# Kernel optimization log

Hardware: AMD Instinct MI355X
Metric: run time of the kernel (lower is better)

The kernel has to match this reference:

```python
import jax, jax.numpy as jnp
import numpy as np

INPUT, LATENT, HIDDEN, LAYERS = 64, 32, 128, 1
N, L = 256, 512


def setup_inputs() -> dict:
    key = jax.random.key(0)
    ks = jax.random.split(key, 12)
    s = 0.02
    inp = {
        "X": jax.random.normal(ks[0], (N, L, INPUT), jnp.float32),
        "eps_z": jax.random.normal(ks[1], (L, LAYERS, N, LATENT), jnp.float32),
        "eps_x": jax.random.normal(ks[2], (L, LAYERS, N, INPUT), jnp.float32),
        # qzcx: NormalModel(input+hidden -> latent): Linear to (mean, raw_std)
        "Wq": s * jax.random.normal(ks[3], (INPUT + HIDDEN, 2 * LATENT), jnp.float32),
        "bq": jnp.zeros((2 * LATENT,), jnp.float32),
        # pxcz: NormalModel(latent+hidden -> input)
        "Wp": s * jax.random.normal(ks[4], (LATENT + HIDDEN, 2 * INPUT), jnp.float32),
        "bp": jnp.zeros((2 * INPUT,), jnp.float32),
        # GRUCell(input+latent -> hidden), gates ordered (r, z, n) as in torch
        "W_ih": s * jax.random.normal(ks[5], (INPUT + LATENT, 3 * HIDDEN), jnp.float32),
        "W_hh": s * jax.random.normal(ks[6], (HIDDEN, 3 * HIDDEN), jnp.float32),
        "b_ih": jnp.zeros((3 * HIDDEN,), jnp.float32),
        "b_hh": jnp.zeros((3 * HIDDEN,), jnp.float32),
    }
    return inp


def _normal(x, W, b):
    # Linear head producing (mean, std) with softplus-positive std
    out = x @ W + b
    mean, raw = jnp.split(out, 2, axis=-1)
    return mean, jax.nn.softplus(raw)


def _gru(xcat, h, W_ih, W_hh, b_ih, b_hh):
    gi = xcat @ W_ih + b_ih
    gh = h @ W_hh + b_hh
    gi_r, gi_z, gi_n = jnp.split(gi, 3, axis=-1)
    gh_r, gh_z, gh_n = jnp.split(gh, 3, axis=-1)
    r = jax.nn.sigmoid(gi_r + gh_r)
    z = jax.nn.sigmoid(gi_z + gh_z)
    n = jnp.tanh(gi_n + r * gh_n)
    return (1.0 - z) * n + z * h


def reference(X, eps_z, eps_x, Wq, bq, Wp, bp, W_ih, W_hh, b_ih, b_hh):
    # X: [N, L, input] (batch_first). Recurrence over L via lax.scan.
    Xt = jnp.transpose(X, (1, 0, 2))  # [L, N, input]

    def cell(x, h, ez, ex):
        # one VRNNCell step (eval path); x:[N,In], h:[N,H]
        inf_mean, inf_std = _normal(jnp.concatenate([x, h], -1), Wq, bq)
        z_gen = inf_mean + inf_std * ez  # rsample
        x_mean, x_std = _normal(jnp.concatenate([z_gen, h], -1), Wp, bp)
        x_gen = x_mean + x_std * ex  # rsample
        return _gru(jnp.concatenate([x_gen, z_gen], -1), h, W_ih, W_hh, b_ih, b_hh)

    cell_layers = jax.vmap(cell, in_axes=(None, 0, 0, 0))  # over layer dim

    def step(hs, inputs):
        x, ez, ex = inputs
        new_hs = cell_layers(x, hs, ez, ex)  # [LAYERS, N, H]
        return new_hs, new_hs[-1]

    h0 = jnp.zeros((LAYERS, X.shape[0], HIDDEN), X.dtype)
    hs_final, outs = jax.lax.scan(step, h0, (Xt, eps_z, eps_x))
    output = jnp.transpose(outs, (1, 0, 2))  # [N, L, H] (batch_first)
    return output, hs_final
```

## Files before the change

### kernel.cpp

```cpp
#include <hip/hip_runtime.h>

namespace {

constexpr int NROWS = 256, LSTEPS = 512, IN = 64, LAT = 32, HID = 128;

typedef _Float16 h2 __attribute__((ext_vector_type(2)));
typedef _Float16 h8 __attribute__((ext_vector_type(8)));

__device__ __forceinline__ float fast_sigmoid(float x) {
    return __fdividef(1.f, 1.f + __expf(-x));
}
__device__ __forceinline__ float fast_softplus(float x) {
    return fmaxf(x, 0.f) + log1pf(__expf(-fabsf(x)));
}
__device__ __forceinline__ float fast_tanh(float x) {
    float e = __expf(-2.f * fabsf(x));
    float t = __fdividef(1.f - e, 1.f + e);
    return copysignf(t, x);
}

__device__ __forceinline__ float dot2f(h2 w, h2 a, float c) {
#if __has_builtin(__builtin_amdgcn_fdot2)
    return __builtin_amdgcn_fdot2(w, a, c, false);
#else
    return fmaf((float)w[0], (float)a[0], fmaf((float)w[1], (float)a[1], c));
#endif
}

__device__ __forceinline__ h2 packw(float a, float b) {
    h2 r; r[0] = (_Float16)a; r[1] = (_Float16)b; return r;
}

template<int BASE, int NPAIR>
__device__ __forceinline__ float dotp2(const _Float16* act, const h2 (&w)[120]) {
    float a0 = 0.f, a1 = 0.f, a2 = 0.f, a3 = 0.f;
#pragma unroll
    for (int i = 0; i < NPAIR / 4; ++i) {
        h8 blk = *(const h8*)(act + 8 * i);
        a0 = dot2f(w[BASE + 4 * i + 0], __builtin_shufflevector(blk, blk, 0, 1), a0);
        a1 = dot2f(w[BASE + 4 * i + 1], __builtin_shufflevector(blk, blk, 2, 3), a1);
        a2 = dot2f(w[BASE + 4 * i + 2], __builtin_shufflevector(blk, blk, 4, 5), a2);
        a3 = dot2f(w[BASE + 4 * i + 3], __builtin_shufflevector(blk, blk, 6, 7), a3);
    }
    return (a0 + a1) + (a2 + a3);
}

}

__global__ __launch_bounds__(512)
__attribute__((amdgpu_waves_per_eu(2, 2)))
void vrnn_kernel(
    const float* __restrict__ X, const float* __restrict__ EZ, const float* __restrict__ EX,
    const float* __restrict__ Wq, const float* __restrict__ bq,
    const float* __restrict__ Wp, const float* __restrict__ bp,
    const float* __restrict__ Wih, const float* __restrict__ Whh,
    const float* __restrict__ bih, const float* __restrict__ bhh,
    float* __restrict__ out)
{
    __shared__ alignas(16) _Float16 XH[192];
    __shared__ alignas(16) _Float16 ZH[160];
    __shared__ alignas(16) _Float16 XZ[96];
    __shared__ alignas(16) float q_part[64][4];
    __shared__ alignas(16) float p_part[128][2];
    __shared__ alignas(16) float gi_part[384][2];
    __shared__ alignas(16) float gh_part[384][2];

    const int t = threadIdx.x;
    const int n = blockIdx.x;

    h2 wpk[120];

    if (t < 256) {
        {
            const int m = t >> 2, k0 = (t & 3) * 48;
#pragma unroll
            for (int j = 0; j < 24; ++j) { int k = k0 + 2 * j;
                wpk[j] = packw(Wq[k * 64 + m], Wq[(k + 1) * 64 + m]); }
        }
        {
            const int m = t >> 1, k0 = (t & 1) * 80;
#pragma unroll
            for (int j = 0; j < 40; ++j) { int k = k0 + 2 * j;
                wpk[24 + j] = packw(Wp[k * 128 + m], Wp[(k + 1) * 128 + m]); }
        }
        {
            const int m = t;
#pragma unroll
            for (int j = 0; j < 48; ++j) { int k = 2 * j;
                wpk[64 + j] = packw(Wih[k * 384 + m], Wih[(k + 1) * 384 + m]); }
        }
    } else {
        const int y = t - 256;
        const int mo = y >> 1, k0 = (y & 1) * 64;
#pragma unroll
        for (int s = 0; s < 3; ++s) {
            const int m = s * 128 + mo;
#pragma unroll
            for (int j = 0; j < 32; ++j) { int k = k0 + 2 * j;
                wpk[s * 32 + j] = packw(Whh[k * 384 + m], Whh[(k + 1) * 384 + m]); }
        }
        {
            const int m = 256 + mo, kg = (y & 1) * 48;
#pragma unroll
            for (int j = 0; j < 24; ++j) { int k = kg + 2 * j;
                wpk[96 + j] = packw(Wih[k * 384 + m], Wih[(k + 1) * 384 + m]); }
        }
    }

    float bz0 = 0.f, bz1 = 0.f, bx0 = 0.f, bx1 = 0.f;
    float bir = 0.f, biz = 0.f, bin_ = 0.f, bhr = 0.f, bhz = 0.f, bhn = 0.f;
    if (t < 32)  { bz0 = bq[t]; bz1 = bq[t + 32]; }
    if (t < 64)  { bx0 = bp[t]; bx1 = bp[t + 64]; }
    if (t < 128) { bir = bih[t]; biz = bih[128 + t]; bin_ = bih[256 + t];
                   bhr = bhh[t]; bhz = bhh[128 + t]; bhn = bhh[256 + t]; }

    const float* Xrow = X + n * (LSTEPS * IN);
    float* orow = out + n * (LSTEPS * HID);
    float hreg = 0.f;
    if (t < 128) { XH[64 + t] = (_Float16)0.f; ZH[32 + t] = (_Float16)0.f; }
    if (t < 64)  XH[t] = (_Float16)Xrow[t];
    float ez_nxt = (t < 32) ? EZ[n * LAT + t] : 0.f;
    float ex_nxt = (t < 64) ? EX[n * IN + t]  : 0.f;
    float xn_nxt = 0.f;
    __syncthreads();

    for (int l = 0; l < LSTEPS; ++l) {
        const float ez_cur = ez_nxt, ex_cur = ex_nxt;
        if (l + 1 < LSTEPS) {
            if (t < 32) ez_nxt = EZ[(l + 1) * (NROWS * LAT) + n * LAT + t];
            if (t < 64) { ex_nxt = EX[(l + 1) * (NROWS * IN) + n * IN + t];
                          xn_nxt = Xrow[(l + 1) * IN + t]; }
        }

        if (t < 256) {
            const int m = t >> 2, ks = t & 3;
            q_part[m][ks] = dotp2<0, 24>(XH + ks * 48, wpk);
        } else {
            const int y = t - 256;
            gh_part[y >> 1][y & 1] = dotp2<0, 32>(XH + 64 + (y & 1) * 64, wpk);
        }
        __syncthreads();

        if (t < 32) {
            float4 qm = *(const float4*)q_part[t];
            float4 qr = *(const float4*)q_part[t + 32];
            float mean = (qm.x + qm.y) + (qm.z + qm.w) + bz0;
            float raw  = (qr.x + qr.y) + (qr.z + qr.w) + bz1;
            float z = fmaf(fast_softplus(raw), ez_cur, mean);
            ZH[t] = (_Float16)z; XZ[64 + t] = (_Float16)z;
        }
        __syncthreads();

        if (t < 256) {
            const int m = t >> 1, ks = t & 1;
            p_part[m][ks] = dotp2<24, 40>(ZH + ks * 80, wpk);
        } else {
            const int y = t - 256;
            gh_part[128 + (y >> 1)][y & 1] = dotp2<32, 32>(XH + 64 + (y & 1) * 64, wpk);
        }
        __syncthreads();

        if (t < 64) {
            float mean = p_part[t][0] + p_part[t][1] + bx0;
            float raw  = p_part[t + 64][0] + p_part[t + 64][1] + bx1;
            float xg = fmaf(fast_softplus(raw), ex_cur, mean);
            XZ[t] = (_Float16)xg;
        }
        __syncthreads();

        if (t < 256) {
            gi_part[t][0] = dotp2<64, 48>(XZ, wpk);
            if (t < 64 && l + 1 < LSTEPS) XH[t] = (_Float16)xn_nxt;
        } else {
            const int y = t - 256;
            gh_part[256 + (y >> 1)][y & 1] = dotp2<64, 32>(XH + 64 + (y & 1) * 64, wpk);
            gi_part[256 + (y >> 1)][y & 1] = dotp2<96, 24>(XZ + (y & 1) * 48, wpk);
        }
        __syncthreads();

        if (t < 128) {
            float gir = gi_part[t][0] + bir;
            float giz = gi_part[128 + t][0] + biz;
            float gin = gi_part[256 + t][0] + gi_part[256 + t][1] + bin_;
            float ghr = gh_part[t][0] + gh_part[t][1] + bhr;
            float ghz = gh_part[128 + t][0] + gh_part[128 + t][1] + bhz;
            float ghn = gh_part[256 + t][0] + gh_part[256 + t][1] + bhn;
            float r  = fast_sigmoid(gir + ghr);
            float zg = fast_sigmoid(giz + ghz);
            float nn = fast_tanh(fmaf(r, ghn, gin));
            float hnew = fmaf(zg, hreg - nn, nn);
            hreg = hnew;
            _Float16 hf = (_Float16)hnew;
            XH[64 + t] = hf; ZH[32 + t] = hf;
            orow[l * HID + t] = hnew;
        }
        __syncthreads();
    }

    if (t < 128) out[NROWS * LSTEPS * HID + n * HID + t] = hreg;
}

extern "C" void kernel_launch(void* const* d_in, const int* in_sizes, int n_in,
                              void* d_out, int out_size, void* d_ws, size_t ws_size,
                              hipStream_t stream) {
    const float* X   = (const float*)d_in[0];
    const float* EZ  = (const float*)d_in[1];
    const float* EX  = (const float*)d_in[2];
    const float* Wq  = (const float*)d_in[3];
    const float* bq  = (const float*)d_in[4];
    const float* Wp  = (const float*)d_in[5];
    const float* bp  = (const float*)d_in[6];
    const float* Wih = (const float*)d_in[7];
    const float* Whh = (const float*)d_in[8];
    const float* bih = (const float*)d_in[9];
    const float* bhh = (const float*)d_in[10];
    float* out = (float*)d_out;

    vrnn_kernel<<<dim3(NROWS), dim3(512), 0, stream>>>(
        X, EZ, EX, Wq, bq, Wp, bp, Wih, Whh, bih, bhh, out);
}
```

Before: 952.1 us.

## Reassign per-thread work to cut barriers and reduce heads via wave shuffles

Redistributes the weight slices across the 512 threads so the W_hh product is split evenly between both halves, and the h-part of the p-head is computed early alongside q. The q and p head reductions now use __shfl_xor inside a wave instead of shared-memory partial arrays, which removes two of the six barriers per timestep. The GRU input gates are split by the z and x contributions so they can be computed in separate phases. In exchange, gate accumulation needs more partial sums per output and the register-resident weight mapping becomes more complex.

```diff
diff --git a/kernel.cpp b/kernel.cpp
--- a/kernel.cpp
+++ b/kernel.cpp
@@ -32,15 +32,15 @@
 }
 
 template<int BASE, int NPAIR>
-__device__ __forceinline__ float dotp2(const _Float16* act, const h2 (&w)[120]) {
-    float a0 = 0.f, a1 = 0.f, a2 = 0.f, a3 = 0.f;
+__device__ __forceinline__ float dotp2(const _Float16* act, const h2 (&w)[120], float init) {
+    float a0 = init, a1 = 0.f, a2 = 0.f, a3 = 0.f;
 #pragma unroll
     for (int i = 0; i < NPAIR / 4; ++i) {
-        h8 blk = *(const h8*)(act + 8 * i);
-        a0 = dot2f(w[BASE + 4 * i + 0], __builtin_shufflevector(blk, blk, 0, 1), a0);
-        a1 = dot2f(w[BASE + 4 * i + 1], __builtin_shufflevector(blk, blk, 2, 3), a1);
-        a2 = dot2f(w[BASE + 4 * i + 2], __builtin_shufflevector(blk, blk, 4, 5), a2);
-        a3 = dot2f(w[BASE + 4 * i + 3], __builtin_shufflevector(blk, blk, 6, 7), a3);
+        h8 b = *(const h8*)(act + 8 * i);
+        a0 = dot2f(w[BASE + 4 * i + 0], __builtin_shufflevector(b, b, 0, 1), a0);
+        a1 = dot2f(w[BASE + 4 * i + 1], __builtin_shufflevector(b, b, 2, 3), a1);
+        a2 = dot2f(w[BASE + 4 * i + 2], __builtin_shufflevector(b, b, 4, 5), a2);
+        a3 = dot2f(w[BASE + 4 * i + 3], __builtin_shufflevector(b, b, 6, 7), a3);
     }
     return (a0 + a1) + (a2 + a3);
 }
@@ -58,140 +58,178 @@
     float* __restrict__ out)
 {
     __shared__ alignas(16) _Float16 XH[192];
-    __shared__ alignas(16) _Float16 ZH[160];
-    __shared__ alignas(16) _Float16 XZ[96];
-    __shared__ alignas(16) float q_part[64][4];
-    __shared__ alignas(16) float p_part[128][2];
-    __shared__ alignas(16) float gi_part[384][2];
-    __shared__ alignas(16) float gh_part[384][2];
+    __shared__ alignas(16) _Float16 ZH[32];
+    __shared__ alignas(16) _Float16 XZ[64];
+    __shared__ alignas(16) float gh_part[384][4];
+    __shared__ alignas(16) float gi_part[384][8];
 
     const int t = threadIdx.x;
     const int n = blockIdx.x;
 
     h2 wpk[120];
 
+    const int y = t - 256;
+
+    int mg[3], kqg[3];
+    int mx[3], kqx[3];
+    int mz[3], khz[3];
+#pragma unroll
+    for (int i = 0; i < 3; ++i) {
+        int s = (t < 256) ? (3 * t + i) : (768 + 3 * y + i);
+        mg[i] = s >> 2; kqg[i] = s & 3;
+        mx[i] = s >> 2; kqx[i] = s & 3;
+        if (t >= 256) { int sz = 3 * y + i; mz[i] = sz >> 1; khz[i] = sz & 1; }
+        else { mz[i] = 0; khz[i] = 0; }
+    }
+
     if (t < 256) {
-        {
-            const int m = t >> 2, k0 = (t & 3) * 48;
-#pragma unroll
-            for (int j = 0; j < 24; ++j) { int k = k0 + 2 * j;
-                wpk[j] = packw(Wq[k * 64 + m], Wq[(k + 1) * 64 + m]); }
-        }
-        {
-            const int m = t >> 1, k0 = (t & 1) * 80;
-#pragma unroll
-            for (int j = 0; j < 40; ++j) { int k = k0 + 2 * j;
-                wpk[24 + j] = packw(Wp[k * 128 + m], Wp[(k + 1) * 128 + m]); }
-        }
-        {
-            const int m = t;
-#pragma unroll
-            for (int j = 0; j < 48; ++j) { int k = 2 * j;
-                wpk[64 + j] = packw(Wih[k * 384 + m], Wih[(k + 1) * 384 + m]); }
-        }
+        const int j = t >> 2, sub = t & 3;
+        const int o = (sub < 2) ? j : j + 64;
+        const int kh = sub & 1;
+#pragma unroll
+        for (int p = 0; p < 32; ++p) { int k = 32 + 64 * kh + 2 * p;
+            wpk[p] = packw(Wp[k * 128 + o], Wp[(k + 1) * 128 + o]); }
+#pragma unroll
+        for (int p = 0; p < 8; ++p) { int k = 16 * kh + 2 * p;
+            wpk[32 + p] = packw(Wp[k * 128 + o], Wp[(k + 1) * 128 + o]); }
+#pragma unroll
+        for (int i = 0; i < 3; ++i)
+#pragma unroll
+            for (int p = 0; p < 16; ++p) { int k = 32 * kqg[i] + 2 * p;
+                wpk[40 + 16 * i + p] = packw(Whh[k * 384 + mg[i]], Whh[(k + 1) * 384 + mg[i]]); }
+#pragma unroll
+        for (int i = 0; i < 3; ++i)
+#pragma unroll
+            for (int p = 0; p < 8; ++p) { int k = 16 * kqx[i] + 2 * p;
+                wpk[88 + 8 * i + p] = packw(Wih[k * 384 + mx[i]], Wih[(k + 1) * 384 + mx[i]]); }
     } else {
-        const int y = t - 256;
-        const int mo = y >> 1, k0 = (y & 1) * 64;
-#pragma unroll
-        for (int s = 0; s < 3; ++s) {
-            const int m = s * 128 + mo;
-#pragma unroll
-            for (int j = 0; j < 32; ++j) { int k = k0 + 2 * j;
-                wpk[s * 32 + j] = packw(Whh[k * 384 + m], Whh[(k + 1) * 384 + m]); }
-        }
-        {
-            const int m = 256 + mo, kg = (y & 1) * 48;
-#pragma unroll
-            for (int j = 0; j < 24; ++j) { int k = kg + 2 * j;
-                wpk[96 + j] = packw(Wih[k * 384 + m], Wih[(k + 1) * 384 + m]); }
-        }
-    }
-
-    float bz0 = 0.f, bz1 = 0.f, bx0 = 0.f, bx1 = 0.f;
+        const int j = y >> 3, sub = y & 7;
+        const int o = (sub < 4) ? j : j + 32;
+        const int k0 = (sub & 3) * 48;
+#pragma unroll
+        for (int p = 0; p < 24; ++p) { int k = k0 + 2 * p;
+            wpk[p] = packw(Wq[k * 64 + o], Wq[(k + 1) * 64 + o]); }
+#pragma unroll
+        for (int i = 0; i < 3; ++i)
+#pragma unroll
+            for (int p = 0; p < 16; ++p) { int k = 32 * kqg[i] + 2 * p;
+                wpk[24 + 16 * i + p] = packw(Whh[k * 384 + mg[i]], Whh[(k + 1) * 384 + mg[i]]); }
+#pragma unroll
+        for (int i = 0; i < 3; ++i)
+#pragma unroll
+            for (int p = 0; p < 8; ++p) { int k = 64 + 16 * khz[i] + 2 * p;
+                wpk[72 + 8 * i + p] = packw(Wih[k * 384 + mz[i]], Wih[(k + 1) * 384 + mz[i]]); }
+#pragma unroll
+        for (int i = 0; i < 3; ++i)
+#pragma unroll
+            for (int p = 0; p < 8; ++p) { int k = 16 * kqx[i] + 2 * p;
+                wpk[96 + 8 * i + p] = packw(Wih[k * 384 + mx[i]], Wih[(k + 1) * 384 + mx[i]]); }
+    }
+
+    float bqm = 0.f, bqr = 0.f, bpm = 0.f, bpr = 0.f;
     float bir = 0.f, biz = 0.f, bin_ = 0.f, bhr = 0.f, bhz = 0.f, bhn = 0.f;
-    if (t < 32)  { bz0 = bq[t]; bz1 = bq[t + 32]; }
-    if (t < 64)  { bx0 = bp[t]; bx1 = bp[t + 64]; }
+    if (t >= 256 && (y & 7) == 0) { bqm = bq[y >> 3]; bqr = bq[(y >> 3) + 32]; }
+    if (t < 256 && (t & 3) == 0)  { bpm = bp[t >> 2]; bpr = bp[(t >> 2) + 64]; }
     if (t < 128) { bir = bih[t]; biz = bih[128 + t]; bin_ = bih[256 + t];
                    bhr = bhh[t]; bhz = bhh[128 + t]; bhn = bhh[256 + t]; }
 
     const float* Xrow = X + n * (LSTEPS * IN);
     float* orow = out + n * (LSTEPS * HID);
     float hreg = 0.f;
-    if (t < 128) { XH[64 + t] = (_Float16)0.f; ZH[32 + t] = (_Float16)0.f; }
+    if (t < 128) XH[64 + t] = (_Float16)0.f;
     if (t < 64)  XH[t] = (_Float16)Xrow[t];
-    float ez_nxt = (t < 32) ? EZ[n * LAT + t] : 0.f;
-    float ex_nxt = (t < 64) ? EX[n * IN + t]  : 0.f;
-    float xn_nxt = 0.f;
+
+    float ez_nxt = 0.f, ex_nxt = 0.f, xn_nxt = 0.f;
+    if (t >= 256 && (y & 7) == 0) ez_nxt = EZ[n * LAT + (y >> 3)];
+    if (t < 256 && (t & 3) == 0)  ex_nxt = EX[n * IN + (t >> 2)];
     __syncthreads();
+
+    float ph = 0.f;
 
     for (int l = 0; l < LSTEPS; ++l) {
         const float ez_cur = ez_nxt, ex_cur = ex_nxt;
         if (l + 1 < LSTEPS) {
-            if (t < 32) ez_nxt = EZ[(l + 1) * (NROWS * LAT) + n * LAT + t];
-            if (t < 64) { ex_nxt = EX[(l + 1) * (NROWS * IN) + n * IN + t];
-                          xn_nxt = Xrow[(l + 1) * IN + t]; }
+            if (t >= 256 && (y & 7) == 0) ez_nxt = EZ[(l + 1) * (NROWS * LAT) + n * LAT + (y >> 3)];
+            if (t < 256 && (t & 3) == 0)  ex_nxt = EX[(l + 1) * (NROWS * IN) + n * IN + (t >> 2)];
+            if (t < 64) xn_nxt = Xrow[(l + 1) * IN + t];
         }
 
         if (t < 256) {
-            const int m = t >> 2, ks = t & 3;
-            q_part[m][ks] = dotp2<0, 24>(XH + ks * 48, wpk);
+            const int kh = t & 1;
+            ph = dotp2<0, 32>(XH + 64 + 64 * kh, wpk, 0.f);
+            float g0 = dotp2<40, 16>(XH + 64 + 32 * kqg[0], wpk, 0.f);
+            float g1 = dotp2<56, 16>(XH + 64 + 32 * kqg[1], wpk, 0.f);
+            float g2 = dotp2<72, 16>(XH + 64 + 32 * kqg[2], wpk, 0.f);
+            gh_part[mg[0]][kqg[0]] = g0;
+            gh_part[mg[1]][kqg[1]] = g1;
+            gh_part[mg[2]][kqg[2]] = g2;
         } else {
-            const int y = t - 256;
-            gh_part[y >> 1][y & 1] = dotp2<0, 32>(XH + 64 + (y & 1) * 64, wpk);
-        }
-        __syncthreads();
-
-        if (t < 32) {
-            float4 qm = *(const float4*)q_part[t];
-            float4 qr = *(const float4*)q_part[t + 32];
-            float mean = (qm.x + qm.y) + (qm.z + qm.w) + bz0;
-            float raw  = (qr.x + qr.y) + (qr.z + qr.w) + bz1;
-            float z = fmaf(fast_softplus(raw), ez_cur, mean);
-            ZH[t] = (_Float16)z; XZ[64 + t] = (_Float16)z;
+            const int sub = y & 7, k0 = (sub & 3) * 48;
+            float q = dotp2<0, 24>(XH + k0, wpk, 0.f);
+            float g0 = dotp2<24, 16>(XH + 64 + 32 * kqg[0], wpk, 0.f);
+            float g1 = dotp2<40, 16>(XH + 64 + 32 * kqg[1], wpk, 0.f);
+            float g2 = dotp2<56, 16>(XH + 64 + 32 * kqg[2], wpk, 0.f);
+            gh_part[mg[0]][kqg[0]] = g0;
+            gh_part[mg[1]][kqg[1]] = g1;
+            gh_part[mg[2]][kqg[2]] = g2;
+            q += __shfl_xor(q, 1);
+            q += __shfl_xor(q, 2);
+            float other = __shfl_xor(q, 4);
+            if (sub == 0) {
+                float z = (q + bqm) + fast_softplus(other + bqr) * ez_cur;
+                ZH[y >> 3] = (_Float16)z;
+            }
         }
         __syncthreads();
 
         if (t < 256) {
-            const int m = t >> 1, ks = t & 1;
-            p_part[m][ks] = dotp2<24, 40>(ZH + ks * 80, wpk);
+            const int kh = t & 1, sub = t & 3;
+            float tot = dotp2<32, 8>(ZH + 16 * kh, wpk, ph);
+            tot += __shfl_xor(tot, 1);
+            float other = __shfl_xor(tot, 2);
+            if (sub == 0) {
+                float xg = (tot + bpm) + fast_softplus(other + bpr) * ex_cur;
+                XZ[t >> 2] = (_Float16)xg;
+            }
         } else {
-            const int y = t - 256;
-            gh_part[128 + (y >> 1)][y & 1] = dotp2<32, 32>(XH + 64 + (y & 1) * 64, wpk);
-        }
-        __syncthreads();
-
-        if (t < 64) {
-            float mean = p_part[t][0] + p_part[t][1] + bx0;
-            float raw  = p_part[t + 64][0] + p_part[t + 64][1] + bx1;
-            float xg = fmaf(fast_softplus(raw), ex_cur, mean);
-            XZ[t] = (_Float16)xg;
+            gi_part[mz[0]][khz[0]] = dotp2<72, 8>(ZH + 16 * khz[0], wpk, 0.f);
+            gi_part[mz[1]][khz[1]] = dotp2<80, 8>(ZH + 16 * khz[1], wpk, 0.f);
+            gi_part[mz[2]][khz[2]] = dotp2<88, 8>(ZH + 16 * khz[2], wpk, 0.f);
         }
         __syncthreads();
 
         if (t < 256) {
-            gi_part[t][0] = dotp2<64, 48>(XZ, wpk);
+            gi_part[mx[0]][2 + kqx[0]] = dotp2<88, 8>(XZ + 16 * kqx[0], wpk, 0.f);
+            gi_part[mx[1]][2 + kqx[1]] = dotp2<96, 8>(XZ + 16 * kqx[1], wpk, 0.f);
+            gi_part[mx[2]][2 + kqx[2]] = dotp2<104, 8>(XZ + 16 * kqx[2], wpk, 0.f);
             if (t < 64 && l + 1 < LSTEPS) XH[t] = (_Float16)xn_nxt;
         } else {
-            const int y = t - 256;
-            gh_part[256 + (y >> 1)][y & 1] = dotp2<64, 32>(XH + 64 + (y & 1) * 64, wpk);
-            gi_part[256 + (y >> 1)][y & 1] = dotp2<96, 24>(XZ + (y & 1) * 48, wpk);
+            gi_part[mx[0]][2 + kqx[0]] = dotp2<96, 8>(XZ + 16 * kqx[0], wpk, 0.f);
+            gi_part[mx[1]][2 + kqx[1]] = dotp2<104, 8>(XZ + 16 * kqx[1], wpk, 0.f);
+            gi_part[mx[2]][2 + kqx[2]] = dotp2<112, 8>(XZ + 16 * kqx[2], wpk, 0.f);
         }
         __syncthreads();
 
         if (t < 128) {
-            float gir = gi_part[t][0] + bir;
-            float giz = gi_part[128 + t][0] + biz;
-            float gin = gi_part[256 + t][0] + gi_part[256 + t][1] + bin_;
-            float ghr = gh_part[t][0] + gh_part[t][1] + bhr;
-            float ghz = gh_part[128 + t][0] + gh_part[128 + t][1] + bhz;
-            float ghn = gh_part[256 + t][0] + gh_part[256 + t][1] + bhn;
+            float4 a; float2 b2;
+            a = *(const float4*)&gi_part[t][0];        b2 = *(const float2*)&gi_part[t][4];
+            float gir = (a.x + a.y) + (a.z + a.w) + (b2.x + b2.y) + bir;
+            a = *(const float4*)&gi_part[128 + t][0];  b2 = *(const float2*)&gi_part[128 + t][4];
+            float giz = (a.x + a.y) + (a.z + a.w) + (b2.x + b2.y) + biz;
+            a = *(const float4*)&gi_part[256 + t][0];  b2 = *(const float2*)&gi_part[256 + t][4];
+            float gin = (a.x + a.y) + (a.z + a.w) + (b2.x + b2.y) + bin_;
+            a = *(const float4*)&gh_part[t][0];
+            float ghr = (a.x + a.y) + (a.z + a.w) + bhr;
+            a = *(const float4*)&gh_part[128 + t][0];
+            float ghz = (a.x + a.y) + (a.z + a.w) + bhz;
+            a = *(const float4*)&gh_part[256 + t][0];
+            float ghn = (a.x + a.y) + (a.z + a.w) + bhn;
             float r  = fast_sigmoid(gir + ghr);
             float zg = fast_sigmoid(giz + ghz);
             float nn = fast_tanh(fmaf(r, ghn, gin));
             float hnew = fmaf(zg, hreg - nn, nn);
             hreg = hnew;
-            _Float16 hf = (_Float16)hnew;
-            XH[64 + t] = hf; ZH[32 + t] = hf;
+            XH[64 + t] = (_Float16)hnew;
             orow[l * HID + t] = hnew;
         }
         __syncthreads();
```

After: 1.023 ms. 1.07x slower.

## Split VRNN step across 1024 threads with shuffle reductions and fewer barriers

Applied to the files above, without the earlier changes.

Doubles the block to 1024 threads and repartitions the per-step work. One half computes the hidden-to-hidden GRU products, while the other half computes the q, p and input-gate products, splitting the p and gi dot products into h-dependent and z/x-dependent parts so they can overlap. Partial sums are reduced with cross-lane shuffles instead of shared-memory staging arrays, which cuts the barriers per step from six to four. It also swaps __syncthreads for a raw s_waitcnt+s_barrier and uses a cheaper softplus log. The risk is higher register pressure with 1024 threads, and the hand-written barrier relies on its lgkmcnt wait to order the shared-memory writes.

```diff
diff --git a/kernel.cpp b/kernel.cpp
--- a/kernel.cpp
+++ b/kernel.cpp
@@ -11,45 +11,48 @@
     return __fdividef(1.f, 1.f + __expf(-x));
 }
 __device__ __forceinline__ float fast_softplus(float x) {
-    return fmaxf(x, 0.f) + log1pf(__expf(-fabsf(x)));
+    return fmaxf(x, 0.f) + __logf(1.f + __expf(-fabsf(x)));
 }
 __device__ __forceinline__ float fast_tanh(float x) {
     float e = __expf(-2.f * fabsf(x));
-    float t = __fdividef(1.f - e, 1.f + e);
-    return copysignf(t, x);
-}
-
-__device__ __forceinline__ float dot2f(h2 w, h2 a, float c) {
-#if __has_builtin(__builtin_amdgcn_fdot2)
+    return copysignf(__fdividef(1.f - e, 1.f + e), x);
+}
+__device__ __forceinline__ float dot2(h2 w, h2 a, float c) {
     return __builtin_amdgcn_fdot2(w, a, c, false);
-#else
-    return fmaf((float)w[0], (float)a[0], fmaf((float)w[1], (float)a[1], c));
-#endif
-}
-
+}
 __device__ __forceinline__ h2 packw(float a, float b) {
     h2 r; r[0] = (_Float16)a; r[1] = (_Float16)b; return r;
 }
-
-template<int BASE, int NPAIR>
-__device__ __forceinline__ float dotp2(const _Float16* act, const h2 (&w)[120]) {
-    float a0 = 0.f, a1 = 0.f, a2 = 0.f, a3 = 0.f;
-#pragma unroll
-    for (int i = 0; i < NPAIR / 4; ++i) {
-        h8 blk = *(const h8*)(act + 8 * i);
-        a0 = dot2f(w[BASE + 4 * i + 0], __builtin_shufflevector(blk, blk, 0, 1), a0);
-        a1 = dot2f(w[BASE + 4 * i + 1], __builtin_shufflevector(blk, blk, 2, 3), a1);
-        a2 = dot2f(w[BASE + 4 * i + 2], __builtin_shufflevector(blk, blk, 4, 5), a2);
-        a3 = dot2f(w[BASE + 4 * i + 3], __builtin_shufflevector(blk, blk, 6, 7), a3);
-    }
-    return (a0 + a1) + (a2 + a3);
-}
-
-}
-
-__global__ __launch_bounds__(512)
-__attribute__((amdgpu_waves_per_eu(2, 2)))
-void vrnn_kernel(
+__device__ __forceinline__ void soft_barrier() {
+    asm volatile("s_waitcnt lgkmcnt(0)\n\ts_barrier" ::: "memory");
+}
+template<int NB>
+__device__ __forceinline__ void load_acts(const _Float16* p, h2* o) {
+#pragma unroll
+    for (int i = 0; i < NB; ++i) {
+        h8 b = *(const h8*)(p + 8 * i);
+        o[4*i+0] = __builtin_shufflevector(b, b, 0, 1);
+        o[4*i+1] = __builtin_shufflevector(b, b, 2, 3);
+        o[4*i+2] = __builtin_shufflevector(b, b, 4, 5);
+        o[4*i+3] = __builtin_shufflevector(b, b, 6, 7);
+    }
+}
+template<int NP>
+__device__ __forceinline__ float dotw(const h2* w, const h2* a, float init) {
+    float s0 = init, s1 = 0.f, s2 = 0.f, s3 = 0.f;
+#pragma unroll
+    for (int i = 0; i < NP / 4; ++i) {
+        s0 = dot2(w[4*i+0], a[4*i+0], s0);
+        s1 = dot2(w[4*i+1], a[4*i+1], s1);
+        s2 = dot2(w[4*i+2], a[4*i+2], s2);
+        s3 = dot2(w[4*i+3], a[4*i+3], s3);
+    }
+    return (s0 + s1) + (s2 + s3);
+}
+
+}
+
+__global__ __launch_bounds__(1024) void vrnn_kernel(
     const float* __restrict__ X, const float* __restrict__ EZ, const float* __restrict__ EX,
     const float* __restrict__ Wq, const float* __restrict__ bq,
     const float* __restrict__ Wp, const float* __restrict__ bp,
@@ -58,146 +61,168 @@
     float* __restrict__ out)
 {
     __shared__ alignas(16) _Float16 XH[192];
-    __shared__ alignas(16) _Float16 ZH[160];
-    __shared__ alignas(16) _Float16 XZ[96];
-    __shared__ alignas(16) float q_part[64][4];
-    __shared__ alignas(16) float p_part[128][2];
-    __shared__ alignas(16) float gi_part[384][2];
-    __shared__ alignas(16) float gh_part[384][2];
-
-    const int t = threadIdx.x;
-    const int n = blockIdx.x;
-
-    h2 wpk[120];
-
-    if (t < 256) {
-        {
-            const int m = t >> 2, k0 = (t & 3) * 48;
-#pragma unroll
-            for (int j = 0; j < 24; ++j) { int k = k0 + 2 * j;
-                wpk[j] = packw(Wq[k * 64 + m], Wq[(k + 1) * 64 + m]); }
-        }
-        {
-            const int m = t >> 1, k0 = (t & 1) * 80;
-#pragma unroll
-            for (int j = 0; j < 40; ++j) { int k = k0 + 2 * j;
-                wpk[24 + j] = packw(Wp[k * 128 + m], Wp[(k + 1) * 128 + m]); }
-        }
-        {
-            const int m = t;
-#pragma unroll
-            for (int j = 0; j < 48; ++j) { int k = 2 * j;
-                wpk[64 + j] = packw(Wih[k * 384 + m], Wih[(k + 1) * 384 + m]); }
+    __shared__ alignas(16) _Float16 ZH[32];
+    __shared__ alignas(16) _Float16 XZ[64];
+    __shared__ alignas(16) float GIR[128][4];
+
+    const int t = threadIdx.x, n = blockIdx.x;
+    const bool isG = (t < 512);
+    const int e = t - 512;
+
+    h2 wpk[80];
+
+    float bh0=0,bh1=0,bh2=0,bi0=0,bi1=0,bi2=0;
+    float bqm=0,bqr=0,bpm=0,bpr=0;
+    float hprev = 0.f;
+
+    if (isG) {
+        const int u = t >> 2, q = t & 3;
+#pragma unroll
+        for (int g = 0; g < 3; ++g)
+#pragma unroll
+            for (int p = 0; p < 16; ++p) {
+                int k = 32*q + 2*p;
+                wpk[g*16+p] = packw(Whh[k*384 + g*128 + u], Whh[(k+1)*384 + g*128 + u]);
+            }
+        if (q == 0) {
+            bh0 = bhh[u]; bh1 = bhh[128+u]; bh2 = bhh[256+u];
+            bi0 = bih[u]; bi1 = bih[128+u]; bi2 = bih[256+u];
         }
     } else {
-        const int y = t - 256;
-        const int mo = y >> 1, k0 = (y & 1) * 64;
-#pragma unroll
-        for (int s = 0; s < 3; ++s) {
-            const int m = s * 128 + mo;
-#pragma unroll
-            for (int j = 0; j < 32; ++j) { int k = k0 + 2 * j;
-                wpk[s * 32 + j] = packw(Whh[k * 384 + m], Whh[(k + 1) * 384 + m]); }
-        }
-        {
-            const int m = 256 + mo, kg = (y & 1) * 48;
-#pragma unroll
-            for (int j = 0; j < 24; ++j) { int k = kg + 2 * j;
-                wpk[96 + j] = packw(Wih[k * 384 + m], Wih[(k + 1) * 384 + m]); }
-        }
-    }
-
-    float bz0 = 0.f, bz1 = 0.f, bx0 = 0.f, bx1 = 0.f;
-    float bir = 0.f, biz = 0.f, bin_ = 0.f, bhr = 0.f, bhz = 0.f, bhn = 0.f;
-    if (t < 32)  { bz0 = bq[t]; bz1 = bq[t + 32]; }
-    if (t < 64)  { bx0 = bp[t]; bx1 = bp[t + 64]; }
-    if (t < 128) { bir = bih[t]; biz = bih[128 + t]; bin_ = bih[256 + t];
-                   bhr = bhh[t]; bhz = bhh[128 + t]; bhn = bhh[256 + t]; }
-
-    const float* Xrow = X + n * (LSTEPS * IN);
-    float* orow = out + n * (LSTEPS * HID);
-    float hreg = 0.f;
-    if (t < 128) { XH[64 + t] = (_Float16)0.f; ZH[32 + t] = (_Float16)0.f; }
-    if (t < 64)  XH[t] = (_Float16)Xrow[t];
-    float ez_nxt = (t < 32) ? EZ[n * LAT + t] : 0.f;
-    float ex_nxt = (t < 64) ? EX[n * IN + t]  : 0.f;
-    float xn_nxt = 0.f;
+        const int lane8 = e & 7, mr = (e >> 2) & 1, kq = e & 3;
+        const int xu8 = e >> 3, gu = e >> 2;
+        const int o = xu8 + mr * 64;
+#pragma unroll
+        for (int p = 0; p < 16; ++p) { int k = 32 + 32*kq + 2*p;
+            wpk[p] = packw(Wp[k*128+o], Wp[(k+1)*128+o]); }
+#pragma unroll
+        for (int p = 0; p < 4; ++p) { int k = 8*kq + 2*p;
+            wpk[16+p] = packw(Wp[k*128+o], Wp[(k+1)*128+o]); }
+#pragma unroll
+        for (int g = 0; g < 3; ++g) {
+#pragma unroll
+            for (int p = 0; p < 8; ++p) { int k = 16*kq + 2*p;
+                wpk[20+g*8+p] = packw(Wih[k*384+g*128+gu], Wih[(k+1)*384+g*128+gu]); }
+#pragma unroll
+            for (int p = 0; p < 4; ++p) { int k = 64 + 8*kq + 2*p;
+                wpk[44+g*4+p] = packw(Wih[k*384+g*128+gu], Wih[(k+1)*384+g*128+gu]); }
+        }
+        if (lane8 == 0) { bpm = bp[xu8]; bpr = bp[64+xu8]; }
+        if (e < 256) {
+            const int zu8 = e >> 3, oq = zu8 + mr*32;
+#pragma unroll
+            for (int p = 0; p < 24; ++p) { int k = 48*kq + 2*p;
+                wpk[56+p] = packw(Wq[k*64+oq], Wq[(k+1)*64+oq]); }
+            if (lane8 == 0) { bqm = bq[zu8]; bqr = bq[32+zu8]; }
+        }
+    }
+
+    const float* Xrow = X + (size_t)n * LSTEPS * IN;
+    float* orow = out + (size_t)n * LSTEPS * HID + (t >> 2);
+    const int ei = isG ? 0 : e;
+    const float* ezq = EZ + n*LAT + (ei >> 3);
+    const float* exq = EX + n*IN + (ei >> 3);
+    float ez=0, ex=0, ezn=0, exn=0, xnA=0, xnB=0;
+    if (!isG && e < 256 && (e & 7) == 0) ez = ezq[0];
+    if (!isG && (e & 7) == 0) ex = exq[0];
+    ezq += NROWS * LAT; exq += NROWS * IN;
+    if (t < 128) XH[64 + t] = (_Float16)0.f;
+    if (t < 64) { XH[t] = (_Float16)Xrow[t]; xnA = Xrow[IN + t]; }
     __syncthreads();
 
+    float gh0=0, gh1=0, gh2=0, ph=0, giz0=0, giz1=0, giz2=0;
+
     for (int l = 0; l < LSTEPS; ++l) {
-        const float ez_cur = ez_nxt, ex_cur = ex_nxt;
-        if (l + 1 < LSTEPS) {
-            if (t < 32) ez_nxt = EZ[(l + 1) * (NROWS * LAT) + n * LAT + t];
-            if (t < 64) { ex_nxt = EX[(l + 1) * (NROWS * IN) + n * IN + t];
-                          xn_nxt = Xrow[(l + 1) * IN + t]; }
-        }
-
-        if (t < 256) {
-            const int m = t >> 2, ks = t & 3;
-            q_part[m][ks] = dotp2<0, 24>(XH + ks * 48, wpk);
+        if (isG) {
+            if (t < 64 && l + 2 < LSTEPS) xnB = Xrow[(size_t)(l + 2) * IN + t];
+        } else if ((e & 7) == 0) {
+            if (l + 1 < LSTEPS) {
+                if (e < 256) ezn = ezq[0];
+                exn = exq[0];
+            }
+            ezq += NROWS * LAT; exq += NROWS * IN;
+        }
+
+        if (isG) {
+            const int q = t & 3;
+            h2 av[16]; load_acts<4>(XH + 64 + 32*q, av);
+            gh0 = dotw<16>(wpk +  0, av, 0.f);
+            gh1 = dotw<16>(wpk + 16, av, 0.f);
+            gh2 = dotw<16>(wpk + 32, av, 0.f);
         } else {
-            const int y = t - 256;
-            gh_part[y >> 1][y & 1] = dotp2<0, 32>(XH + 64 + (y & 1) * 64, wpk);
-        }
-        __syncthreads();
-
-        if (t < 32) {
-            float4 qm = *(const float4*)q_part[t];
-            float4 qr = *(const float4*)q_part[t + 32];
-            float mean = (qm.x + qm.y) + (qm.z + qm.w) + bz0;
-            float raw  = (qr.x + qr.y) + (qr.z + qr.w) + bz1;
-            float z = fmaf(fast_softplus(raw), ez_cur, mean);
-            ZH[t] = (_Float16)z; XZ[64 + t] = (_Float16)z;
-        }
-        __syncthreads();
-
-        if (t < 256) {
-            const int m = t >> 1, ks = t & 1;
-            p_part[m][ks] = dotp2<24, 40>(ZH + ks * 80, wpk);
+            const int kq = e & 3;
+            h2 av[16]; load_acts<4>(XH + 64 + 32*kq, av);
+            ph = dotw<16>(wpk, av, 0.f);
+            if (e < 256) {
+                h2 aq[24]; load_acts<6>(XH + 48*kq, aq);
+                float qd = dotw<24>(wpk + 56, aq, 0.f);
+                qd += __shfl_xor(qd, 1);
+                qd += __shfl_xor(qd, 2);
+                float other = __shfl_xor(qd, 4);
+                if ((e & 7) == 0) {
+                    float z = (qd + bqm) + fast_softplus(other + bqr) * ez;
+                    ZH[e >> 3] = (_Float16)z;
+                }
+            }
+        }
+        soft_barrier();
+
+        if (isG) {
+            if (t < 64 && l + 1 < LSTEPS) XH[t] = (_Float16)xnA;
         } else {
-            const int y = t - 256;
-            gh_part[128 + (y >> 1)][y & 1] = dotp2<32, 32>(XH + 64 + (y & 1) * 64, wpk);
-        }
-        __syncthreads();
-
-        if (t < 64) {
-            float mean = p_part[t][0] + p_part[t][1] + bx0;
-            float raw  = p_part[t + 64][0] + p_part[t + 64][1] + bx1;
-            float xg = fmaf(fast_softplus(raw), ex_cur, mean);
-            XZ[t] = (_Float16)xg;
-        }
-        __syncthreads();
-
-        if (t < 256) {
-            gi_part[t][0] = dotp2<64, 48>(XZ, wpk);
-            if (t < 64 && l + 1 < LSTEPS) XH[t] = (_Float16)xn_nxt;
+            const int kq = e & 3;
+            h2 az[4]; load_acts<1>(ZH + 8*kq, az);
+            float tot = dotw<4>(wpk + 16, az, ph);
+            tot += __shfl_xor(tot, 1);
+            tot += __shfl_xor(tot, 2);
+            float other = __shfl_xor(tot, 4);
+            if ((e & 7) == 0) {
+                float xg = (tot + bpm) + fast_softplus(other + bpr) * ex;
+                XZ[e >> 3] = (_Float16)xg;
+            }
+            giz0 = dotw<4>(wpk + 44, az, 0.f);
+            giz1 = dotw<4>(wpk + 48, az, 0.f);
+            giz2 = dotw<4>(wpk + 52, az, 0.f);
+        }
+        soft_barrier();
+
+        if (isG) {
+            gh0 += __shfl_xor(gh0, 1); gh0 += __shfl_xor(gh0, 2);
+            gh1 += __shfl_xor(gh1, 1); gh1 += __shfl_xor(gh1, 2);
+            gh2 += __shfl_xor(gh2, 1); gh2 += __shfl_xor(gh2, 2);
         } else {
-            const int y = t - 256;
-            gh_part[256 + (y >> 1)][y & 1] = dotp2<64, 32>(XH + 64 + (y & 1) * 64, wpk);
-            gi_part[256 + (y >> 1)][y & 1] = dotp2<96, 24>(XZ + (y & 1) * 48, wpk);
-        }
-        __syncthreads();
-
-        if (t < 128) {
-            float gir = gi_part[t][0] + bir;
-            float giz = gi_part[128 + t][0] + biz;
-            float gin = gi_part[256 + t][0] + gi_part[256 + t][1] + bin_;
-            float ghr = gh_part[t][0] + gh_part[t][1] + bhr;
-            float ghz = gh_part[128 + t][0] + gh_part[128 + t][1] + bhz;
-            float ghn = gh_part[256 + t][0] + gh_part[256 + t][1] + bhn;
-            float r  = fast_sigmoid(gir + ghr);
-            float zg = fast_sigmoid(giz + ghz);
-            float nn = fast_tanh(fmaf(r, ghn, gin));
-            float hnew = fmaf(zg, hreg - nn, nn);
-            hreg = hnew;
-            _Float16 hf = (_Float16)hnew;
-            XH[64 + t] = hf; ZH[32 + t] = hf;
-            orow[l * HID + t] = hnew;
-        }
-        __syncthreads();
-    }
-
-    if (t < 128) out[NROWS * LSTEPS * HID + n * HID + t] = hreg;
+            const int c = e & 3;
+            h2 ax[8]; load_acts<2>(XZ + 16*c, ax);
+            float g0 = dotw<8>(wpk + 20, ax, giz0);
+            float g1 = dotw<8>(wpk + 28, ax, giz1);
+            float g2 = dotw<8>(wpk + 36, ax, giz2);
+            g0 += __shfl_xor(g0, 1); g0 += __shfl_xor(g0, 2);
+            g1 += __shfl_xor(g1, 1); g1 += __shfl_xor(g1, 2);
+            g2 += __shfl_xor(g2, 1); g2 += __shfl_xor(g2, 2);
+            if (c == 0) {
+                float4 v; v.x = g0; v.y = g1; v.z = g2; v.w = 0.f;
+                *(float4*)&GIR[e >> 2][0] = v;
+            }
+        }
+        soft_barrier();
+
+        if (isG && (t & 3) == 0) {
+            const int u = t >> 2;
+            float4 gi = *(const float4*)&GIR[u][0];
+            float rr = fast_sigmoid((gi.x + bi0) + (gh0 + bh0));
+            float zg = fast_sigmoid((gi.y + bi1) + (gh1 + bh1));
+            float nn = fast_tanh(fmaf(rr, gh2 + bh2, gi.z + bi2));
+            float h = fmaf(zg, hprev - nn, nn);
+            hprev = h;
+            XH[64 + u] = (_Float16)h;
+            orow[(size_t)l * HID] = h;
+        }
+        ez = ezn; ex = exn; xnA = xnB;
+        soft_barrier();
+    }
+
+    if (isG && (t & 3) == 0)
+        out[(size_t)NROWS * LSTEPS * HID + (size_t)n * HID + (t >> 2)] = hprev;
 }
 
 extern "C" void kernel_launch(void* const* d_in, const int* in_sizes, int n_in,
@@ -216,6 +241,6 @@
     const float* bhh = (const float*)d_in[10];
     float* out = (float*)d_out;
 
-    vrnn_kernel<<<dim3(NROWS), dim3(512), 0, stream>>>(
+    vrnn_kernel<<<dim3(NROWS), dim3(1024), 0, stream>>>(
         X, EZ, EX, Wq, bq, Wp, bp, Wih, Whh, bih, bhh, out);
 }
```

Result: slower. 2.767 ms (+190.7%).
